# Optimization experiments

Measured on AMD Instinct MI355X. Metric: run time of the kernel, lower is better.

Reference implementation:

```python
import jax, jax.numpy as jnp
import numpy as np

NUM_HEADS = 8
BLOCK = 8      # block_size
HALO = 2       # kernel_size (halo width)


def _rel_to_abs(rel):
    # halo-style relative->absolute conversion
    # rel: [B, G, qh, qw, 2*p-1] -> [B, G, qh, qw, p]
    B, G, qh, qw, dim = rel.shape
    p = (dim + 1) // 2
    gap = p - qw
    flat = rel.reshape(B, G, qh, qw * dim)[:, :, :, qw - 1:-1]
    return flat.reshape(B, G, qh, qw, 2 * (p - 1))[:, :, :, :, gap:p + gap]


def _relative_logits(pos_q, pos_emb_h, pos_emb_w):
    # pos_q: [B, G, qb, qb, kd]; pos_emb_*: [kd, 2*p-1]
    rel_w = _rel_to_abs(jnp.einsum('bghwd,dr->bghwr', pos_q, pos_emb_w))  # [B,G,qb,qb,p] key-width
    q_t = pos_q.transpose(0, 1, 3, 2, 4)
    rel_h = _rel_to_abs(jnp.einsum('bgwhd,dr->bgwhr', q_t, pos_emb_h))
    rel_h = rel_h.transpose(0, 1, 3, 2, 4)  # [B,G,qb,qb,p] key-height
    return rel_h[..., :, None] + rel_w[..., None, :]  # [B,G,qb,qb,p,p]


def reference(x, w_q, w_kv, w_out, pos_emb_h, pos_emb_w):
    B, H, W, C = x.shape
    kd = C // NUM_HEADS                # per-head key dim
    kvk = BLOCK + 2 * HALO             # halo window size
    out_ch = w_out.shape[1]
    v_dim = out_ch // NUM_HEADS
    kv_per_head = (C + out_ch) // NUM_HEADS
    hh, ww = H // BLOCK, W // BLOCK
    scale = float(1.0 / np.sqrt(kd))

    # ---- query (1x1 conv == matmul), blockify ----
    q = (x @ w_q).reshape(B, hh, BLOCK, ww, BLOCK, NUM_HEADS, kd)
    q = q.transpose(0, 5, 1, 3, 2, 4, 6)  # [B,nh,hh,ww,qb,qb,kd]
    attn_q = q.reshape(B, NUM_HEADS, hh, ww, BLOCK * BLOCK, kd) * scale
    pos_q = q.reshape(B, NUM_HEADS * hh * ww, BLOCK, BLOCK, kd)

    # ---- key/value: 1x1 conv, halo pad, unfold into overlapping windows ----
    kv = jnp.pad(x @ w_kv, ((0, 0), (HALO, HALO), (HALO, HALO), (0, 0)))
    idx = np.arange(hh)[:, None] * BLOCK + np.arange(kvk)[None, :]  # [hh,kvk]
    idy = np.arange(ww)[:, None] * BLOCK + np.arange(kvk)[None, :]  # [ww,kvk]
    patches = kv[:, idx][:, :, :, idy]           # [B,hh,kvk,ww,kvk,kv_dim]
    patches = patches.transpose(0, 1, 3, 2, 4, 5)  # [B,hh,ww,kvk,kvk,kv_dim]
    kvh = patches.reshape(B, hh, ww, kvk, kvk, NUM_HEADS, kv_per_head)
    kvh = kvh.transpose(0, 5, 1, 2, 3, 4, 6).reshape(B, NUM_HEADS, hh, ww, kvk * kvk, kv_per_head)
    key, value = kvh[..., :kd], kvh[..., kd:]

    # ---- attention with relative position bias ----
    scores = jnp.einsum('bnhwqd,bnhwkd->bnhwqk', attn_q, key)
    pos = _relative_logits(pos_q, pos_emb_h, pos_emb_w)
    pos = pos.reshape(B, NUM_HEADS, hh, ww, BLOCK * BLOCK, kvk * kvk)
    attn = jax.nn.softmax(scores + pos, axis=-1)
    out = jnp.einsum('bnhwqk,bnhwkv->bnhwqv', attn, value)  # [B,nh,hh,ww,qb*qb,v_dim]

    # ---- de-blockify, output projection ----
    out = out.reshape(B, NUM_HEADS, hh, ww, BLOCK, BLOCK, v_dim)
    out = out.transpose(0, 2, 4, 3, 5, 1, 6).reshape(B, H, W, NUM_HEADS * v_dim)
    return out @ w_out


def setup_inputs() -> dict:
    key = jax.random.key(0)
    ks = jax.random.split(key, 6)
    B, H, W, C = 4, 128, 128, 256
    out_ch = 256
    kd = C // NUM_HEADS
    kvk = BLOCK + 2 * HALO
    std = kd ** -0.5
    return {
        'x': jax.random.normal(ks[0], (B, H, W, C), jnp.float32),
        'w_q': jax.random.normal(ks[1], (C, C), jnp.float32) * 0.02,
        'w_kv': jax.random.normal(ks[2], (C, C + out_ch), jnp.float32) * 0.02,
        'w_out': jax.random.normal(ks[3], (C, out_ch), jnp.float32) * 0.02,
        'pos_emb_h': jax.random.normal(ks[4], (kd, 2 * kvk - 1), jnp.float32) * std,
        'pos_emb_w': jax.random.normal(ks[5], (kd, 2 * kvk - 1), jnp.float32) * std,
    }
```

## Files before the change

### kernel.cpp

```cpp
#include <hip/hip_runtime.h>
#include <hip/hip_bf16.h>
#include <cstdint>


#define KVK 12
#define NKEYS 144
#define VT_S 160
#define PT_S 168
#define LOG2E 1.4426950408889634f

typedef unsigned int u32;
typedef unsigned short u16;
typedef __attribute__((ext_vector_type(8))) __bf16 bf16x8;
typedef __attribute__((ext_vector_type(4))) float f32x4;

__device__ __forceinline__ u16 f2bf(float f) {
    u32 x = __float_as_uint(f);
    return (u16)((x + 0x7fffu + ((x >> 16) & 1u)) >> 16);
}
__device__ __forceinline__ u32 cvtpk(float lo, float hi) {
    u32 d;
    asm("v_cvt_pk_bf16_f32 %0, %1, %2" : "=v"(d) : "v"(lo), "v"(hi));
    return d;
}
__device__ __forceinline__ float max3f(float a, float b, float c) {
    float d;
    asm("v_max3_f32 %0, %1, %2, %3" : "=v"(d) : "v"(a), "v"(b), "v"(c));
    return d;
}
__device__ __forceinline__ float exp2a(float x) {
    float d;
    asm("v_exp_f32 %0, %1" : "=v"(d) : "v"(x));
    return d;
}
__device__ __forceinline__ void gload16(const void* g, void* l) {
    __builtin_amdgcn_global_load_lds(
        (const __attribute__((address_space(1))) void*)g,
        (__attribute__((address_space(3))) void*)l, 16, 0, 0);
}

__global__ __launch_bounds__(256) void prep_weights(const float* __restrict__ wq,
                                                    const float* __restrict__ wkv,
                                                    const float* __restrict__ wout,
                                                    u16* __restrict__ wT,
                                                    u16* __restrict__ woutT,
                                                    const float* __restrict__ emb_h,
                                                    const float* __restrict__ emb_w,
                                                    u16* __restrict__ embT) {
    int blk = blockIdx.x, t = threadIdx.x;
    if (blk < 256) {
        int idx = blk * 256 + t; int nn = idx >> 8, k = idx & 255;
        wT[idx] = f2bf(wq[(long)k * 256 + nn]);
    } else if (blk < 768) {
        int idx = (blk - 256) * 256 + t; int nn = idx >> 8, k = idx & 255;
        float v = wkv[(long)k * 512 + nn];
        if ((nn & 32) == 0) v *= 0.2550348642f;
        wT[65536 + idx] = f2bf(v);
    } else if (blk < 1024) {
        int idx = (blk - 768) * 256 + t; int nn = idx >> 8, k = idx & 255;
        woutT[idx] = f2bf(wout[(long)k * 256 + nn]);
    } else if (blk == 1024) {
        for (int i = t; i < 736; i += 256) {
            int p = i >> 5, d = i & 31;
            embT[i] = f2bf(emb_h[d * 23 + p]);
        }
    } else {
        for (int i = t; i < 736; i += 256) {
            int p = i >> 5, d = i & 31;
            embT[736 + i] = f2bf(emb_w[d * 23 + p]);
        }
    }
}

__global__ __launch_bounds__(256) void gemm_qkv(const float* __restrict__ X,
                                                const u16* __restrict__ WT,
                                                u16* __restrict__ Qb,
                                                u16* __restrict__ KVb) {
    __shared__ u16 As[4096];
    __shared__ u16 Bs[4096];
    const int t = threadIdx.x;
    const int w = t >> 6, lane = t & 63;
    const long m0 = (long)blockIdx.x * 128;
    const long n0 = (long)blockIdx.y * 128;
    const int wr = w >> 1, wc = w & 1;
    const int r = lane & 15, g = lane >> 4;

    f32x4 acc[4][4];
    #pragma unroll
    for (int i = 0; i < 4; ++i)
        #pragma unroll
        for (int j = 0; j < 4; ++j) acc[i][j] = (f32x4){0.f, 0.f, 0.f, 0.f};

    const int rowA0 = t >> 2, csA = (t & 3) * 8;
    const int rowA1 = rowA0 + 64;
    const float* Xg0 = X + (m0 + rowA0) * 256 + csA;
    const float* Xg1 = X + (m0 + rowA1) * 256 + csA;
    const int u0 = w * 128 + lane;
    const int rowB0 = u0 >> 2, csB0 = (u0 & 3) * 8;
    const int u1 = u0 + 64;
    const int rowB1 = u1 >> 2, csB1 = (u1 & 3) * 8;
    const u16* Bg0 = WT + (n0 + rowB0) * 256 + csB0;
    const u16* Bg1 = WT + (n0 + rowB1) * 256 + csB1;
    u16* BsW = &Bs[w * 1024];

    for (int k0 = 0; k0 < 256; k0 += 32) {
        float4 a0 = *reinterpret_cast<const float4*>(Xg0 + k0);
        float4 a1 = *reinterpret_cast<const float4*>(Xg0 + k0 + 4);
        float4 c0 = *reinterpret_cast<const float4*>(Xg1 + k0);
        float4 c1 = *reinterpret_cast<const float4*>(Xg1 + k0 + 4);
        gload16(Bg0 + k0, BsW);
        gload16(Bg1 + k0, BsW + 512);
        uint4 pa, pc;
        pa.x = cvtpk(a0.x, a0.y); pa.y = cvtpk(a0.z, a0.w);
        pa.z = cvtpk(a1.x, a1.y); pa.w = cvtpk(a1.z, a1.w);
        pc.x = cvtpk(c0.x, c0.y); pc.y = cvtpk(c0.z, c0.w);
        pc.z = cvtpk(c1.x, c1.y); pc.w = cvtpk(c1.z, c1.w);
        *reinterpret_cast<uint4*>(&As[rowA0 * 32 + csA]) = pa;
        *reinterpret_cast<uint4*>(&As[rowA1 * 32 + csA]) = pc;
        __syncthreads();
        bf16x8 a[4], b[4];
        #pragma unroll
        for (int i = 0; i < 4; ++i)
            a[i] = *reinterpret_cast<const bf16x8*>(&As[(wr * 64 + i * 16 + r) * 32 + g * 8]);
        #pragma unroll
        for (int j = 0; j < 4; ++j)
            b[j] = *reinterpret_cast<const bf16x8*>(&Bs[(wc * 64 + j * 16 + r) * 32 + g * 8]);
        #pragma unroll
        for (int i = 0; i < 4; ++i)
            #pragma unroll
            for (int j = 0; j < 4; ++j)
                acc[i][j] = __builtin_amdgcn_mfma_f32_16x16x32_bf16(a[i], b[j], acc[i][j], 0, 0, 0);
        __syncthreads();
    }

    const bool isQ = (blockIdx.y < 2);
    #pragma unroll
    for (int i = 0; i < 4; ++i) {
        #pragma unroll
        for (int j = 0; j < 4; ++j) {
            long col = n0 + wc * 64 + j * 16 + r;
            #pragma unroll
            for (int e = 0; e < 4; ++e) {
                long row = m0 + wr * 64 + i * 16 + g * 4 + e;
                u16 v = f2bf(acc[i][j][e]);
                if (isQ) Qb[row * 256 + col] = v;
                else     KVb[row * 512 + col - 256] = v;
            }
        }
    }
}

__global__ __launch_bounds__(256) void mfma_gemm(const u16* __restrict__ A,
                                                 const u16* __restrict__ BT,
                                                 float* __restrict__ C, int N) {
    __shared__ u16 As[4096];
    __shared__ u16 Bs[4096];
    const int t = threadIdx.x;
    const int w = t >> 6, lane = t & 63;
    const long m0 = (long)blockIdx.x * 128;
    const long n0 = (long)blockIdx.y * 128;
    const int wr = w >> 1, wc = w & 1;
    const int r = lane & 15, g = lane >> 4;

    f32x4 acc[4][4];
    #pragma unroll
    for (int i = 0; i < 4; ++i)
        #pragma unroll
        for (int j = 0; j < 4; ++j) acc[i][j] = (f32x4){0.f, 0.f, 0.f, 0.f};

    const int u0 = w * 128 + lane;
    const int row0 = u0 >> 2, cs0 = (u0 & 3) * 8;
    const int u1 = u0 + 64;
    const int row1 = u1 >> 2, cs1 = (u1 & 3) * 8;
    const u16* Ag0 = A + (m0 + row0) * 256 + cs0;
    const u16* Ag1 = A + (m0 + row1) * 256 + cs1;
    const u16* Bg0 = BT + (n0 + row0) * 256 + cs0;
    const u16* Bg1 = BT + (n0 + row1) * 256 + cs1;
    u16* AsW = &As[w * 1024];
    u16* BsW = &Bs[w * 1024];

    for (int k0 = 0; k0 < 256; k0 += 32) {
        gload16(Ag0 + k0, AsW);
        gload16(Ag1 + k0, AsW + 512);
        gload16(Bg0 + k0, BsW);
        gload16(Bg1 + k0, BsW + 512);
        __syncthreads();
        bf16x8 a[4], b[4];
        #pragma unroll
        for (int i = 0; i < 4; ++i)
            a[i] = *reinterpret_cast<const bf16x8*>(&As[(wr * 64 + i * 16 + r) * 32 + g * 8]);
        #pragma unroll
        for (int j = 0; j < 4; ++j)
            b[j] = *reinterpret_cast<const bf16x8*>(&Bs[(wc * 64 + j * 16 + r) * 32 + g * 8]);
        #pragma unroll
        for (int i = 0; i < 4; ++i)
            #pragma unroll
            for (int j = 0; j < 4; ++j)
                acc[i][j] = __builtin_amdgcn_mfma_f32_16x16x32_bf16(a[i], b[j], acc[i][j], 0, 0, 0);
        __syncthreads();
    }

    #pragma unroll
    for (int i = 0; i < 4; ++i)
        #pragma unroll
        for (int j = 0; j < 4; ++j)
            #pragma unroll
            for (int e = 0; e < 4; ++e) {
                long row = m0 + wr * 64 + i * 16 + g * 4 + e;
                long col = n0 + wc * 64 + j * 16 + r;
                C[row * N + col] = acc[i][j][e];
            }
}

__global__ __launch_bounds__(256, 4) void attn_mfma(const u16* __restrict__ Qb,
                                                    const u16* __restrict__ KVb,
                                                    const u16* __restrict__ embT,
                                                    u16* __restrict__ Ob) {
    __shared__ __align__(16) char blob[26624];
    u16* Ks  = (u16*)blob;
    u16* Qe  = (u16*)(blob + 18432);
    u16* ehT = (u16*)(blob + 22528);
    u16* ewT = (u16*)(blob + 24576);
    u16* PT  = (u16*)blob;
    __shared__ u16 Vt[32 * VT_S];

    const int gblk = blockIdx.x;
    const int n = gblk & 7;
    const int bx = (gblk >> 3) & 15;
    const int by = (gblk >> 7) & 15;
    const int b = gblk >> 11;
    const int t = threadIdx.x;
    const int w = t >> 6, lane = t & 63;
    const int g = lane >> 4, r = lane & 15;

    const int q = w * 16 + r;
    const int qi = q >> 3, qj = q & 7;
    const long qrow = ((long)b * 128 + by * 8 + qi) * 128 + bx * 8 + qj;

    bf16x8 qa1 = *reinterpret_cast<const bf16x8*>(Qb + qrow * 256 + n * 32 + g * 8);

    for (int u = t; u < NKEYS * 8; u += 256) {
        int kk = u >> 3, part = u & 7;
        int ky = kk / KVK, kx = kk - ky * KVK;
        int gy = by * 8 + ky - 2, gx = bx * 8 + kx - 2;
        uint4 val = make_uint4(0u, 0u, 0u, 0u);
        if ((unsigned)gy < 128u && (unsigned)gx < 128u) {
            long row = ((long)b * 128 + gy) * 128 + gx;
            val = *reinterpret_cast<const uint4*>(KVb + row * 512 + n * 64 + part * 8);
        }
        if (part < 4) {
            int col = (part * 8) ^ ((kk & 7) << 3);
            *reinterpret_cast<uint4*>(&Ks[kk * 64 + col]) = val;
        } else {
            int d0 = (part - 4) * 8;
            u16 tmp[8];
            *reinterpret_cast<uint4*>(tmp) = val;
            #pragma unroll
            for (int i = 0; i < 8; ++i) {
                int d = d0 + i;
                Vt[d * VT_S + (kk ^ (((d >> 3) & 3) << 3))] = tmp[i];
            }
        }
    }
    for (int u = t; u < 576; u += 256) {
        int kk = u >> 2;
        int col = (32 + (u & 3) * 8) ^ ((kk & 7) << 3);
        *reinterpret_cast<uint4*>(&Ks[kk * 64 + col]) = make_uint4(0u, 0u, 0u, 0u);
    }
    if (t < 64) *reinterpret_cast<uint4*>(&Qe[t * 32 + 24]) = make_uint4(0u, 0u, 0u, 0u);
    if (t >= 224) {
        int d = t - 224;
        int sw = ((d >> 3) & 3) << 3;
        *reinterpret_cast<uint4*>(&Vt[d * VT_S + (144 ^ sw)]) = make_uint4(0u, 0u, 0u, 0u);
        *reinterpret_cast<uint4*>(&Vt[d * VT_S + (152 ^ sw)]) = make_uint4(0u, 0u, 0u, 0u);
    }
    if (t < 184) {
        uint4 v = *reinterpret_cast<const uint4*>(embT + t * 8);
        u16* dst = (t < 92) ? (ehT + t * 8) : (ewT + t * 8 - 736);
        *reinterpret_cast<uint4*>(dst) = v;
    }
    __syncthreads();

    {
        bf16x8 ah0 = *reinterpret_cast<const bf16x8*>(&ehT[r * 32 + g * 8]);
        bf16x8 ah1 = *reinterpret_cast<const bf16x8*>(&ehT[(16 + r) * 32 + g * 8]);
        bf16x8 aw0 = *reinterpret_cast<const bf16x8*>(&ewT[r * 32 + g * 8]);
        bf16x8 aw1 = *reinterpret_cast<const bf16x8*>(&ewT[(16 + r) * 32 + g * 8]);
        f32x4 z = (f32x4){0.f, 0.f, 0.f, 0.f};
        f32x4 rh0 = __builtin_amdgcn_mfma_f32_16x16x32_bf16(ah0, qa1, z, 0, 0, 0);
        f32x4 rh1 = __builtin_amdgcn_mfma_f32_16x16x32_bf16(ah1, qa1, z, 0, 0, 0);
        f32x4 rw0 = __builtin_amdgcn_mfma_f32_16x16x32_bf16(aw0, qa1, z, 0, 0, 0);
        f32x4 rw1 = __builtin_amdgcn_mfma_f32_16x16x32_bf16(aw1, qa1, z, 0, 0, 0);
        #pragma unroll
        for (int ti = 0; ti < 2; ++ti) {
            #pragma unroll
            for (int e = 0; e < 4; ++e) {
                int p = ti * 16 + g * 4 + e;
                float vh = (ti ? rh1[e] : rh0[e]) * LOG2E;
                float vw = (ti ? rw1[e] : rw0[e]) * LOG2E;
                int kyd = p + qi - 11;
                int kxd = p + qj - 11;
                if ((unsigned)kyd < 12u) Qe[q * 32 + kyd] = f2bf(vh);
                if ((unsigned)kxd < 12u) Qe[q * 32 + 12 + kxd] = f2bf(vw);
            }
        }
        if (t < NKEYS) {
            int ky = (t * 171) >> 11;
            int kx = t - 12 * ky;
            int sw = (t & 7) << 3;
            Ks[t * 64 + ((32 + ky) ^ sw)] = 0x3F80;
            Ks[t * 64 + ((44 + kx) ^ sw)] = 0x3F80;
        }
    }
    __syncthreads();

    bf16x8 qa2 = *reinterpret_cast<const bf16x8*>(&Qe[q * 32 + g * 8]);
    f32x4 acc[9];
    #pragma unroll
    for (int j = 0; j < 9; ++j) {
        int krow = j * 16 + r;
        int sw = (r & 7) << 3;
        bf16x8 kb0 = *reinterpret_cast<const bf16x8*>(&Ks[krow * 64 + ((g * 8) ^ sw)]);
        bf16x8 kb1 = *reinterpret_cast<const bf16x8*>(&Ks[krow * 64 + ((32 + g * 8) ^ sw)]);
        f32x4 z = (f32x4){0.f, 0.f, 0.f, 0.f};
        acc[j] = __builtin_amdgcn_mfma_f32_16x16x32_bf16(kb1, qa2,
                 __builtin_amdgcn_mfma_f32_16x16x32_bf16(kb0, qa1, z, 0, 0, 0), 0, 0, 0);
    }

    float mx = max3f(acc[0][0], acc[0][1], acc[0][2]);
    mx = fmaxf(mx, acc[0][3]);
    #pragma unroll
    for (int j = 1; j < 9; ++j)
        mx = max3f(mx, max3f(acc[j][0], acc[j][1], acc[j][2]), acc[j][3]);
    mx = fmaxf(mx, __shfl_xor(mx, 16));
    mx = fmaxf(mx, __shfl_xor(mx, 32));
    float s0 = 0.f, s1 = 0.f, s2 = 0.f, s3 = 0.f;
    u32 pkA[9], pkB[9];
    #pragma unroll
    for (int j = 0; j < 9; ++j) {
        float e0 = exp2a(acc[j][0] - mx);
        float e1 = exp2a(acc[j][1] - mx);
        float e2 = exp2a(acc[j][2] - mx);
        float e3 = exp2a(acc[j][3] - mx);
        s0 += e0; s1 += e1; s2 += e2; s3 += e3;
        pkA[j] = cvtpk(e0, e1);
        pkB[j] = cvtpk(e2, e3);
    }
    float sum = (s0 + s1) + (s2 + s3);
    sum += __shfl_xor(sum, 16);
    sum += __shfl_xor(sum, 32);
    const float inv = __builtin_amdgcn_rcpf(sum);

    __syncthreads();

    {
        const int ptb = q * PT_S;
        #pragma unroll
        for (int j = 0; j < 9; ++j) {
            *reinterpret_cast<u32*>(&PT[ptb + 16 * j + 4 * g]) = pkA[j];
            *reinterpret_cast<u32*>(&PT[ptb + 16 * j + 4 * g + 2]) = pkB[j];
        }
    }
    if (t < 64) {
        *reinterpret_cast<uint4*>(&PT[t * PT_S + 144]) = make_uint4(0u, 0u, 0u, 0u);
        *reinterpret_cast<uint4*>(&PT[t * PT_S + 152]) = make_uint4(0u, 0u, 0u, 0u);
    }
    __syncthreads();

    const int sw0 = (r >> 3) << 3;
    const int sw1 = (2 + (r >> 3)) << 3;
    f32x4 o0 = (f32x4){0.f, 0.f, 0.f, 0.f};
    f32x4 o1 = (f32x4){0.f, 0.f, 0.f, 0.f};
    #pragma unroll
    for (int kk = 0; kk < 5; ++kk) {
        bf16x8 pb = *reinterpret_cast<const bf16x8*>(&PT[q * PT_S + kk * 32 + g * 8]);
        bf16x8 va0 = *reinterpret_cast<const bf16x8*>(&Vt[r * VT_S + ((kk * 32 + g * 8) ^ sw0)]);
        bf16x8 va1 = *reinterpret_cast<const bf16x8*>(&Vt[(16 + r) * VT_S + ((kk * 32 + g * 8) ^ sw1)]);
        o0 = __builtin_amdgcn_mfma_f32_16x16x32_bf16(va0, pb, o0, 0, 0, 0);
        o1 = __builtin_amdgcn_mfma_f32_16x16x32_bf16(va1, pb, o1, 0, 0, 0);
    }
    {
        uint2 st0, st1;
        st0.x = cvtpk(o0[0] * inv, o0[1] * inv);
        st0.y = cvtpk(o0[2] * inv, o0[3] * inv);
        st1.x = cvtpk(o1[0] * inv, o1[1] * inv);
        st1.y = cvtpk(o1[2] * inv, o1[3] * inv);
        *reinterpret_cast<uint2*>(Ob + qrow * 256 + n * 32 + g * 4) = st0;
        *reinterpret_cast<uint2*>(Ob + qrow * 256 + n * 32 + 16 + g * 4) = st1;
    }
}

extern "C" void kernel_launch(void* const* d_in, const int* in_sizes, int n_in,
                              void* d_out, int out_size, void* d_ws, size_t ws_size,
                              hipStream_t stream) {
    const float* x     = (const float*)d_in[0];
    const float* w_q   = (const float*)d_in[1];
    const float* w_kv  = (const float*)d_in[2];
    const float* w_out = (const float*)d_in[3];
    const float* emb_h = (const float*)d_in[4];
    const float* emb_w = (const float*)d_in[5];

    u16* Qb = (u16*)d_out;
    char* ws = (char*)d_ws;
    u16* KVb   = (u16*)(ws);
    u16* Ob    = (u16*)(ws + (size_t)67108864);
    u16* wT    = (u16*)(ws + (size_t)100663296);
    u16* woutT = (u16*)(ws + (size_t)100663296 + 393216);
    u16* embT  = (u16*)(ws + (size_t)100663296 + 524288);

    dim3 blk(256);
    prep_weights<<<dim3(1026), blk, 0, stream>>>(w_q, w_kv, w_out, wT, woutT, emb_h, emb_w, embT);
    gemm_qkv<<<dim3(512, 6), blk, 0, stream>>>(x, wT, Qb, KVb);
    attn_mfma<<<dim3(8192), blk, 0, stream>>>(Qb, KVb, embT, Ob);
    mfma_gemm<<<dim3(512, 2), blk, 0, stream>>>(Ob, woutT, (float*)d_out, 256);
}
```

Before: 160.8 us.

## Stage full X row panel in LDS once and loop over all QKV column tiles

The QKV projection kernel now loads each 128x256 fp32 X panel once, converts it to bf16 and keeps it in LDS with an XOR swizzle. A single block then iterates over all six 128-column output tiles, instead of launching six blocks that each reread and reconverted X. This removes five redundant reads and conversions of the large fp32 input. In exchange it uses 64KB+ of LDS per block, which lowers occupancy, and the launch shrinks to 512 blocks, cutting parallelism and latency hiding.

```diff
diff --git a/kernel.cpp b/kernel.cpp
--- a/kernel.cpp
+++ b/kernel.cpp
@@ -76,75 +76,80 @@
                                                 const u16* __restrict__ WT,
                                                 u16* __restrict__ Qb,
                                                 u16* __restrict__ KVb) {
-    __shared__ u16 As[4096];
+    __shared__ u16 Apan[128 * 256];
     __shared__ u16 Bs[4096];
     const int t = threadIdx.x;
     const int w = t >> 6, lane = t & 63;
     const long m0 = (long)blockIdx.x * 128;
-    const long n0 = (long)blockIdx.y * 128;
     const int wr = w >> 1, wc = w & 1;
     const int r = lane & 15, g = lane >> 4;
 
-    f32x4 acc[4][4];
-    #pragma unroll
-    for (int i = 0; i < 4; ++i)
-        #pragma unroll
-        for (int j = 0; j < 4; ++j) acc[i][j] = (f32x4){0.f, 0.f, 0.f, 0.f};
-
-    const int rowA0 = t >> 2, csA = (t & 3) * 8;
-    const int rowA1 = rowA0 + 64;
-    const float* Xg0 = X + (m0 + rowA0) * 256 + csA;
-    const float* Xg1 = X + (m0 + rowA1) * 256 + csA;
+    #pragma unroll
+    for (int i = 0; i < 16; ++i) {
+        int v = i * 256 + t;
+        int row = v >> 5, u = v & 31;
+        const float* src = X + (m0 + row) * 256 + u * 8;
+        float4 f0 = *reinterpret_cast<const float4*>(src);
+        float4 f1 = *reinterpret_cast<const float4*>(src + 4);
+        uint4 pk;
+        pk.x = cvtpk(f0.x, f0.y); pk.y = cvtpk(f0.z, f0.w);
+        pk.z = cvtpk(f1.x, f1.y); pk.w = cvtpk(f1.z, f1.w);
+        *reinterpret_cast<uint4*>(&Apan[row * 256 + ((u ^ (row & 7)) << 3)]) = pk;
+    }
+
     const int u0 = w * 128 + lane;
     const int rowB0 = u0 >> 2, csB0 = (u0 & 3) * 8;
     const int u1 = u0 + 64;
     const int rowB1 = u1 >> 2, csB1 = (u1 & 3) * 8;
-    const u16* Bg0 = WT + (n0 + rowB0) * 256 + csB0;
-    const u16* Bg1 = WT + (n0 + rowB1) * 256 + csB1;
     u16* BsW = &Bs[w * 1024];
 
-    for (int k0 = 0; k0 < 256; k0 += 32) {
-        float4 a0 = *reinterpret_cast<const float4*>(Xg0 + k0);
-        float4 a1 = *reinterpret_cast<const float4*>(Xg0 + k0 + 4);
-        float4 c0 = *reinterpret_cast<const float4*>(Xg1 + k0);
-        float4 c1 = *reinterpret_cast<const float4*>(Xg1 + k0 + 4);
-        gload16(Bg0 + k0, BsW);
-        gload16(Bg1 + k0, BsW + 512);
-        uint4 pa, pc;
-        pa.x = cvtpk(a0.x, a0.y); pa.y = cvtpk(a0.z, a0.w);
-        pa.z = cvtpk(a1.x, a1.y); pa.w = cvtpk(a1.z, a1.w);
-        pc.x = cvtpk(c0.x, c0.y); pc.y = cvtpk(c0.z, c0.w);
-        pc.z = cvtpk(c1.x, c1.y); pc.w = cvtpk(c1.z, c1.w);
-        *reinterpret_cast<uint4*>(&As[rowA0 * 32 + csA]) = pa;
-        *reinterpret_cast<uint4*>(&As[rowA1 * 32 + csA]) = pc;
-        __syncthreads();
-        bf16x8 a[4], b[4];
+    for (int nt = 0; nt < 6; ++nt) {
+        const long n0 = nt * 128;
+        const u16* Bg0 = WT + (n0 + rowB0) * 256 + csB0;
+        const u16* Bg1 = WT + (n0 + rowB1) * 256 + csB1;
+
+        f32x4 acc[4][4];
         #pragma unroll
         for (int i = 0; i < 4; ++i)
-            a[i] = *reinterpret_cast<const bf16x8*>(&As[(wr * 64 + i * 16 + r) * 32 + g * 8]);
-        #pragma unroll
-        for (int j = 0; j < 4; ++j)
-            b[j] = *reinterpret_cast<const bf16x8*>(&Bs[(wc * 64 + j * 16 + r) * 32 + g * 8]);
-        #pragma unroll
-        for (int i = 0; i < 4; ++i)
+            #pragma unroll
+            for (int j = 0; j < 4; ++j) acc[i][j] = (f32x4){0.f, 0.f, 0.f, 0.f};
+
+        for (int k0 = 0; k0 < 256; k0 += 32) {
+            gload16(Bg0 + k0, BsW);
+            gload16(Bg1 + k0, BsW + 512);
+            __syncthreads();
+            bf16x8 a[4], b[4];
+            const int cu = k0 >> 3;
+            #pragma unroll
+            for (int i = 0; i < 4; ++i) {
+                int row = wr * 64 + i * 16 + r;
+                a[i] = *reinterpret_cast<const bf16x8*>(
+                    &Apan[row * 256 + (((cu + g) ^ (row & 7)) << 3)]);
+            }
             #pragma unroll
             for (int j = 0; j < 4; ++j)
-                acc[i][j] = __builtin_amdgcn_mfma_f32_16x16x32_bf16(a[i], b[j], acc[i][j], 0, 0, 0);
-        __syncthreads();
-    }
-
-    const bool isQ = (blockIdx.y < 2);
-    #pragma unroll
-    for (int i = 0; i < 4; ++i) {
-        #pragma unroll
-        for (int j = 0; j < 4; ++j) {
-            long col = n0 + wc * 64 + j * 16 + r;
-            #pragma unroll
-            for (int e = 0; e < 4; ++e) {
-                long row = m0 + wr * 64 + i * 16 + g * 4 + e;
-                u16 v = f2bf(acc[i][j][e]);
-                if (isQ) Qb[row * 256 + col] = v;
-                else     KVb[row * 512 + col - 256] = v;
+                b[j] = *reinterpret_cast<const bf16x8*>(&Bs[(wc * 64 + j * 16 + r) * 32 + g * 8]);
+            #pragma unroll
+            for (int i = 0; i < 4; ++i)
+                #pragma unroll
+                for (int j = 0; j < 4; ++j)
+                    acc[i][j] = __builtin_amdgcn_mfma_f32_16x16x32_bf16(a[i], b[j], acc[i][j], 0, 0, 0);
+            __syncthreads();
+        }
+
+        const bool isQ = (nt < 2);
+        #pragma unroll
+        for (int i = 0; i < 4; ++i) {
+            #pragma unroll
+            for (int j = 0; j < 4; ++j) {
+                long col = n0 + wc * 64 + j * 16 + r;
+                #pragma unroll
+                for (int e = 0; e < 4; ++e) {
+                    long row = m0 + wr * 64 + i * 16 + g * 4 + e;
+                    u16 v = f2bf(acc[i][j][e]);
+                    if (isQ) Qb[row * 256 + col] = v;
+                    else     KVb[row * 512 + col - 256] = v;
+                }
             }
         }
     }
@@ -410,7 +415,7 @@
 
     dim3 blk(256);
     prep_weights<<<dim3(1026), blk, 0, stream>>>(w_q, w_kv, w_out, wT, woutT, emb_h, emb_w, embT);
-    gemm_qkv<<<dim3(512, 6), blk, 0, stream>>>(x, wT, Qb, KVb);
+    gemm_qkv<<<dim3(512), blk, 0, stream>>>(x, wT, Qb, KVb);
     attn_mfma<<<dim3(8192), blk, 0, stream>>>(Qb, KVb, embT, Ob);
     mfma_gemm<<<dim3(512, 2), blk, 0, stream>>>(Ob, woutT, (float*)d_out, 256);
 }
```

Result: faster. 141.1 us (-12.3%).

## Split QKV GEMM, spill bf16 x once, vectorize transposed-MFMA epilogue stores

Applied to the files above, without the earlier changes.

The fused QKV projection, which re-read and re-converted fp32 x in all six column tiles, is split in two. A Q GEMM over two column tiles also writes a bf16 copy of x from its first tile, and a second bf16 GEMM computes KV from that copy. MFMA operand order is swapped so each lane holds four consecutive columns, letting the epilogues use packed 8-byte bf16 and 16-byte fp32 vector stores instead of scalar stores. This adds an extra launch and a round trip of bf16 x through scratch space in the output buffer.

```diff
diff --git a/kernel.cpp b/kernel.cpp
--- a/kernel.cpp
+++ b/kernel.cpp
@@ -72,10 +72,10 @@
     }
 }
 
-__global__ __launch_bounds__(256) void gemm_qkv(const float* __restrict__ X,
-                                                const u16* __restrict__ WT,
-                                                u16* __restrict__ Qb,
-                                                u16* __restrict__ KVb) {
+__global__ __launch_bounds__(256) void gemm_qx(const float* __restrict__ X,
+                                               const u16* __restrict__ WT,
+                                               u16* __restrict__ Qb,
+                                               u16* __restrict__ xb) {
     __shared__ u16 As[4096];
     __shared__ u16 Bs[4096];
     const int t = threadIdx.x;
@@ -84,6 +84,7 @@
     const long n0 = (long)blockIdx.y * 128;
     const int wr = w >> 1, wc = w & 1;
     const int r = lane & 15, g = lane >> 4;
+    const bool spill = (blockIdx.y == 0);
 
     f32x4 acc[4][4];
     #pragma unroll
@@ -91,10 +92,9 @@
         #pragma unroll
         for (int j = 0; j < 4; ++j) acc[i][j] = (f32x4){0.f, 0.f, 0.f, 0.f};
 
-    const int rowA0 = t >> 2, csA = (t & 3) * 8;
-    const int rowA1 = rowA0 + 64;
-    const float* Xg0 = X + (m0 + rowA0) * 256 + csA;
-    const float* Xg1 = X + (m0 + rowA1) * 256 + csA;
+    const int arow = t >> 1, acol = (t & 1) << 4;
+    const float* Xg = X + (m0 + arow) * 256 + acol;
+    u16* xbg = xb + (m0 + arow) * 256 + acol;
     const int u0 = w * 128 + lane;
     const int rowB0 = u0 >> 2, csB0 = (u0 & 3) * 8;
     const int u1 = u0 + 64;
@@ -104,19 +104,23 @@
     u16* BsW = &Bs[w * 1024];
 
     for (int k0 = 0; k0 < 256; k0 += 32) {
-        float4 a0 = *reinterpret_cast<const float4*>(Xg0 + k0);
-        float4 a1 = *reinterpret_cast<const float4*>(Xg0 + k0 + 4);
-        float4 c0 = *reinterpret_cast<const float4*>(Xg1 + k0);
-        float4 c1 = *reinterpret_cast<const float4*>(Xg1 + k0 + 4);
+        float4 f0 = *reinterpret_cast<const float4*>(Xg + k0);
+        float4 f1 = *reinterpret_cast<const float4*>(Xg + k0 + 4);
+        float4 f2 = *reinterpret_cast<const float4*>(Xg + k0 + 8);
+        float4 f3 = *reinterpret_cast<const float4*>(Xg + k0 + 12);
         gload16(Bg0 + k0, BsW);
         gload16(Bg1 + k0, BsW + 512);
-        uint4 pa, pc;
-        pa.x = cvtpk(a0.x, a0.y); pa.y = cvtpk(a0.z, a0.w);
-        pa.z = cvtpk(a1.x, a1.y); pa.w = cvtpk(a1.z, a1.w);
-        pc.x = cvtpk(c0.x, c0.y); pc.y = cvtpk(c0.z, c0.w);
-        pc.z = cvtpk(c1.x, c1.y); pc.w = cvtpk(c1.z, c1.w);
-        *reinterpret_cast<uint4*>(&As[rowA0 * 32 + csA]) = pa;
-        *reinterpret_cast<uint4*>(&As[rowA1 * 32 + csA]) = pc;
+        uint4 p0, p1;
+        p0.x = cvtpk(f0.x, f0.y); p0.y = cvtpk(f0.z, f0.w);
+        p0.z = cvtpk(f1.x, f1.y); p0.w = cvtpk(f1.z, f1.w);
+        p1.x = cvtpk(f2.x, f2.y); p1.y = cvtpk(f2.z, f2.w);
+        p1.z = cvtpk(f3.x, f3.y); p1.w = cvtpk(f3.z, f3.w);
+        *reinterpret_cast<uint4*>(&As[arow * 32 + acol]) = p0;
+        *reinterpret_cast<uint4*>(&As[arow * 32 + acol + 8]) = p1;
+        if (spill) {
+            *reinterpret_cast<uint4*>(xbg + k0) = p0;
+            *reinterpret_cast<uint4*>(xbg + k0 + 8) = p1;
+        }
         __syncthreads();
         bf16x8 a[4], b[4];
         #pragma unroll
@@ -129,30 +133,28 @@
         for (int i = 0; i < 4; ++i)
             #pragma unroll
             for (int j = 0; j < 4; ++j)
-                acc[i][j] = __builtin_amdgcn_mfma_f32_16x16x32_bf16(a[i], b[j], acc[i][j], 0, 0, 0);
+                acc[i][j] = __builtin_amdgcn_mfma_f32_16x16x32_bf16(b[j], a[i], acc[i][j], 0, 0, 0);
         __syncthreads();
     }
 
-    const bool isQ = (blockIdx.y < 2);
     #pragma unroll
     for (int i = 0; i < 4; ++i) {
+        long row = m0 + wr * 64 + i * 16 + r;
         #pragma unroll
         for (int j = 0; j < 4; ++j) {
-            long col = n0 + wc * 64 + j * 16 + r;
-            #pragma unroll
-            for (int e = 0; e < 4; ++e) {
-                long row = m0 + wr * 64 + i * 16 + g * 4 + e;
-                u16 v = f2bf(acc[i][j][e]);
-                if (isQ) Qb[row * 256 + col] = v;
-                else     KVb[row * 512 + col - 256] = v;
-            }
-        }
-    }
-}
-
+            long colb = n0 + wc * 64 + j * 16 + g * 4;
+            uint2 st;
+            st.x = cvtpk(acc[i][j][0], acc[i][j][1]);
+            st.y = cvtpk(acc[i][j][2], acc[i][j][3]);
+            *reinterpret_cast<uint2*>(Qb + row * 256 + colb) = st;
+        }
+    }
+}
+
+template <int C_BF16>
 __global__ __launch_bounds__(256) void mfma_gemm(const u16* __restrict__ A,
                                                  const u16* __restrict__ BT,
-                                                 float* __restrict__ C, int N) {
+                                                 void* __restrict__ Cv, int N) {
     __shared__ u16 As[4096];
     __shared__ u16 Bs[4096];
     const int t = threadIdx.x;
@@ -196,20 +198,27 @@
         for (int i = 0; i < 4; ++i)
             #pragma unroll
             for (int j = 0; j < 4; ++j)
-                acc[i][j] = __builtin_amdgcn_mfma_f32_16x16x32_bf16(a[i], b[j], acc[i][j], 0, 0, 0);
+                acc[i][j] = __builtin_amdgcn_mfma_f32_16x16x32_bf16(b[j], a[i], acc[i][j], 0, 0, 0);
         __syncthreads();
     }
 
     #pragma unroll
-    for (int i = 0; i < 4; ++i)
-        #pragma unroll
-        for (int j = 0; j < 4; ++j)
-            #pragma unroll
-            for (int e = 0; e < 4; ++e) {
-                long row = m0 + wr * 64 + i * 16 + g * 4 + e;
-                long col = n0 + wc * 64 + j * 16 + r;
-                C[row * N + col] = acc[i][j][e];
+    for (int i = 0; i < 4; ++i) {
+        long row = m0 + wr * 64 + i * 16 + r;
+        #pragma unroll
+        for (int j = 0; j < 4; ++j) {
+            long colb = n0 + wc * 64 + j * 16 + g * 4;
+            if (C_BF16) {
+                uint2 st;
+                st.x = cvtpk(acc[i][j][0], acc[i][j][1]);
+                st.y = cvtpk(acc[i][j][2], acc[i][j][3]);
+                *reinterpret_cast<uint2*>((u16*)Cv + row * N + colb) = st;
+            } else {
+                float4 st = make_float4(acc[i][j][0], acc[i][j][1], acc[i][j][2], acc[i][j][3]);
+                *reinterpret_cast<float4*>((float*)Cv + row * N + colb) = st;
             }
+        }
+    }
 }
 
 __global__ __launch_bounds__(256, 4) void attn_mfma(const u16* __restrict__ Qb,
@@ -401,6 +410,7 @@
     const float* emb_w = (const float*)d_in[5];
 
     u16* Qb = (u16*)d_out;
+    u16* xb = (u16*)((char*)d_out + (size_t)33554432);
     char* ws = (char*)d_ws;
     u16* KVb   = (u16*)(ws);
     u16* Ob    = (u16*)(ws + (size_t)67108864);
@@ -410,7 +420,8 @@
 
     dim3 blk(256);
     prep_weights<<<dim3(1026), blk, 0, stream>>>(w_q, w_kv, w_out, wT, woutT, emb_h, emb_w, embT);
-    gemm_qkv<<<dim3(512, 6), blk, 0, stream>>>(x, wT, Qb, KVb);
+    gemm_qx<<<dim3(512, 2), blk, 0, stream>>>(x, wT, Qb, xb);
+    mfma_gemm<1><<<dim3(512, 4), blk, 0, stream>>>(xb, wT + 65536, KVb, 512);
     attn_mfma<<<dim3(8192), blk, 0, stream>>>(Qb, KVb, embT, Ob);
-    mfma_gemm<<<dim3(512, 2), blk, 0, stream>>>(Ob, woutT, (float*)d_out, 256);
-}
+    mfma_gemm<0><<<dim3(512, 2), blk, 0, stream>>>(Ob, woutT, (float*)d_out, 256);
+}
```

New measurement: 163.9 us. Within noise of the previous version (+1.9%).
